# Optimization experiments

Measured on AMD Instinct MI355X. Metric: run time of the kernel, lower is better.

## Reference

```python
import jax, jax.numpy as jnp
import numpy as np

TEMPERATURE = 0.02
B, T, D = 32, 256, 128


def _l2norm(x):
    return x / jnp.linalg.norm(x, axis=-1, keepdims=True)


def setup_inputs() -> dict:
    key = jax.random.key(0)
    k1, k2, k3, k4, k5, k6 = jax.random.split(key, 6)
    query_single = _l2norm(jax.random.normal(k1, (B, D), dtype=jnp.float32))
    pos_single = _l2norm(jax.random.normal(k2, (B, D), dtype=jnp.float32))
    query_multi = _l2norm(jax.random.normal(k3, (B, T, D), dtype=jnp.float32))
    pos_multi = _l2norm(jax.random.normal(k4, (B, T, D), dtype=jnp.float32))
    # variable-length masks (at least 1 valid token each, like real tokenized batches)
    q_len = jax.random.randint(k5, (B,), T // 4, T + 1)
    p_len = jax.random.randint(k6, (B,), T // 4, T + 1)
    pos = jnp.arange(T)[None, :]
    q_mask = pos < q_len[:, None]
    p_mask = pos < p_len[:, None]
    return {
        "query_single": query_single,
        "pos_single": pos_single,
        "query_multi": query_multi,
        "pos_multi": pos_multi,
        "q_mask": q_mask,
        "p_mask": p_mask,
    }


def _late_interaction_similarity(q_tokens, q_mask, p_tokens, p_mask):
    # All-pairs token similarity: [Bq, Bp, Tq, Tp]
    sim = jnp.einsum("bqd,cpd->bcqp", q_tokens, p_tokens)
    neg = jnp.finfo(sim.dtype).min
    sim = jnp.where(p_mask[None, :, None, :], sim, neg)
    mx = jnp.max(sim, axis=-1)                       # [Bq, Bp, Tq]
    mx = jnp.where(q_mask[:, None, :], mx, 0.0)      # drop invalid query tokens
    s = jnp.sum(mx, axis=-1)                         # [Bq, Bp]
    t_i = jnp.maximum(jnp.sum(q_mask, axis=-1), 1).astype(sim.dtype)  # [Bq]
    return s / t_i[:, None]


def _diag_cross_entropy(logits):
    # labels = arange(B): standard in-batch InfoNCE
    logp = jax.nn.log_softmax(logits, axis=-1)
    return -jnp.mean(jnp.diagonal(logp))


def reference(query_single, pos_single, query_multi, pos_multi, q_mask, p_mask):
    tau = TEMPERATURE
    dense_sim = query_single @ pos_single.T                       # [B, B]
    single_loss = _diag_cross_entropy(dense_sim / tau)

    S_late = _late_interaction_similarity(query_multi, q_mask, pos_multi, p_mask)
    multi_loss = _diag_cross_entropy(S_late / tau)

    dense_probs = jax.nn.softmax(dense_sim / tau, axis=1)
    late_probs = jax.nn.softmax(S_late / tau, axis=1)
    eps = 1e-8
    kl = jnp.mean(jnp.sum(dense_probs * jnp.log((dense_probs + eps) / (late_probs + eps)), axis=1))

    total_loss = single_loss + multi_loss + kl
    return (total_loss, single_loss, multi_loss, kl)
```

## Files before the change

### kernel.cpp

```cpp
#include <hip/hip_runtime.h>
#include <hip/hip_bf16.h>

#define B_SZ 32
#define T_SZ 256
#define D_SZ 128
#define TAU_INV 50.0f

typedef __bf16 bf16x8 __attribute__((ext_vector_type(8)));
typedef float f32x4 __attribute__((ext_vector_type(4)));

__device__ __forceinline__ unsigned short f2bf(float f) {
    union { float f; unsigned int u; } v; v.f = f;
    unsigned int r = v.u + 0x7fffu + ((v.u >> 16) & 1u);
    return (unsigned short)(r >> 16);
}

__device__ __forceinline__ bool mask_is_byte(const void* m) {
    return ((const int*)m)[0] != 1;
}
__device__ __forceinline__ int mget(const void* m, int idx, bool isb) {
    return isb ? (((const unsigned char*)m)[idx] != 0) : (((const int*)m)[idx] != 0);
}

__global__ __launch_bounds__(256) void cvt_prep(
    const float* __restrict__ qsrc, const float* __restrict__ psrc,
    const void* __restrict__ qmask, const void* __restrict__ pmask,
    unsigned short* __restrict__ Qb, unsigned short* __restrict__ Pb,
    float* __restrict__ maddF, float* __restrict__ qmulF,
    int* __restrict__ p_hiA, float* __restrict__ tcntA) {
    const int tid = threadIdx.x;
    const int half = blockIdx.x >> 10;
    if (half < 2) {
        const float* s = half ? psrc : qsrc;
        unsigned short* d = half ? Pb : Qb;
        int i = ((blockIdx.x & 1023) * 256 + tid) * 4;
        float4 v = *(const float4*)(s + i);
        ushort4 o;
        o.x = f2bf(v.x); o.y = f2bf(v.y); o.z = f2bf(v.z); o.w = f2bf(v.w);
        *(ushort4*)(d + i) = o;
        return;
    }
    __shared__ int sl[4], sc[4];
    const bool isb = mask_is_byte(qmask);
    const int r = blockIdx.x - 2048;
    const int t = tid;
    const int pm = mget(pmask, r * T_SZ + t, isb);
    const int qm = mget(qmask, r * T_SZ + t, isb);
    maddF[r * T_SZ + t] = pm ? 0.0f : -1e30f;
    qmulF[r * T_SZ + t] = qm ? 1.0f : 0.0f;
    int lp = pm ? t + 1 : 0, cq = qm;
    #pragma unroll
    for (int off = 1; off < 64; off <<= 1) {
        int o = __shfl_xor(lp, off);
        lp = o > lp ? o : lp;
        cq += __shfl_xor(cq, off);
    }
    if ((tid & 63) == 0) { sl[tid >> 6] = lp; sc[tid >> 6] = cq; }
    __syncthreads();
    if (tid == 0) {
        int LP = sl[0], CQ = sc[0];
        #pragma unroll
        for (int i = 1; i < 4; ++i) { LP = sl[i] > LP ? sl[i] : LP; CQ += sc[i]; }
        p_hiA[r] = LP > 1 ? LP : 1;
        tcntA[r] = (float)(CQ > 1 ? CQ : 1);
    }
}

__global__ __launch_bounds__(512, 4) void late_sim(
    const unsigned short* __restrict__ Qbf, const unsigned short* __restrict__ Pbf,
    const float* __restrict__ maddF, const float* __restrict__ qmulF,
    const int* __restrict__ p_hiA, float* __restrict__ sraw)
{
    __shared__ __align__(16) unsigned char Plds[T_SZ * D_SZ * 2];
    __shared__ float madd[T_SZ];
    __shared__ float qmul[2][T_SZ];
    __shared__ float wsum[2][8];

    const int tid = threadIdx.x;
    const int l   = tid & 63;
    const int w   = tid >> 6;
    const int bid = blockIdx.x;
    const int xcd = bid & 7;
    const int idx = bid >> 3;
    const int bg  = xcd * 2 + (idx >> 5);
    const int c   = idx & 31;
    const int b0  = bg, b1 = bg + 16;
    const int lr  = l & 15;
    const int lg  = l >> 4;

    const int p_hi    = p_hiA[c];
    const int ptmax   = (p_hi + 15) >> 4;
    const int stiters = (p_hi + 31) >> 5;

    const int qrow = w * 32 + (l & 31);
    const bool do0 = __any(qmulF[b0 * T_SZ + qrow] > 0.0f);
    const bool do1 = __any(qmulF[b1 * T_SZ + qrow] > 0.0f);

    bf16x8 qf0[2][4] = {}, qf1[2][4] = {};
    if (do0)
        #pragma unroll
        for (int qt = 0; qt < 2; ++qt)
            #pragma unroll
            for (int k = 0; k < 4; ++k)
                qf0[qt][k] = *(const bf16x8*)(Qbf + b0 * (T_SZ * D_SZ)
                              + (w * 32 + qt * 16 + lr) * D_SZ + k * 32 + lg * 8);
    if (do1)
        #pragma unroll
        for (int qt = 0; qt < 2; ++qt)
            #pragma unroll
            for (int k = 0; k < 4; ++k)
                qf1[qt][k] = *(const bf16x8*)(Qbf + b1 * (T_SZ * D_SZ)
                              + (w * 32 + qt * 16 + lr) * D_SZ + k * 32 + lg * 8);

    {
        const unsigned short* Pc = Pbf + c * (T_SZ * D_SZ);
        for (int it = 0; it < stiters; ++it) {
            int j   = it * 512 + w * 64 + l;
            int row = j >> 4;
            int cj  = j & 15;
            const unsigned short* src = Pc + row * D_SZ + ((cj ^ (row & 7)) << 3);
            __builtin_amdgcn_global_load_lds(
                (const __attribute__((address_space(1))) unsigned int*)src,
                (__attribute__((address_space(3))) unsigned int*)(Plds + (it * 512 + w * 64) * 16),
                16, 0, 0);
        }
    }
    if (tid < 64) {
        *(float4*)(madd + tid * 4) = *(const float4*)(maddF + c * T_SZ + tid * 4);
    } else if (tid < 128) {
        int t = tid - 64;
        *(float4*)(qmul[0] + t * 4) = *(const float4*)(qmulF + b0 * T_SZ + t * 4);
    } else if (tid < 192) {
        int t = tid - 128;
        *(float4*)(qmul[1] + t * 4) = *(const float4*)(qmulF + b1 * T_SZ + t * 4);
    }
    __syncthreads();

    float r00 = -3e38f, r01 = -3e38f, r10 = -3e38f, r11 = -3e38f;

    for (int pt = 0; pt < ptmax; ++pt) {
        f32x4 a00 = {0,0,0,0}, a01 = {0,0,0,0}, a10 = {0,0,0,0}, a11 = {0,0,0,0};
        #pragma unroll
        for (int k = 0; k < 4; ++k) {
            int row = pt * 16 + lr;
            bf16x8 af = *(const bf16x8*)(Plds + row * 256 + (((k * 4 + lg) ^ (row & 7)) << 4));
            if (do0) {
                a00 = __builtin_amdgcn_mfma_f32_16x16x32_bf16(af, qf0[0][k], a00, 0, 0, 0);
                a01 = __builtin_amdgcn_mfma_f32_16x16x32_bf16(af, qf0[1][k], a01, 0, 0, 0);
            }
            if (do1) {
                a10 = __builtin_amdgcn_mfma_f32_16x16x32_bf16(af, qf1[0][k], a10, 0, 0, 0);
                a11 = __builtin_amdgcn_mfma_f32_16x16x32_bf16(af, qf1[1][k], a11, 0, 0, 0);
            }
        }
        float pm0 = madd[pt * 16 + lg * 4 + 0];
        float pm1 = madd[pt * 16 + lg * 4 + 1];
        float pm2 = madd[pt * 16 + lg * 4 + 2];
        float pm3v = madd[pt * 16 + lg * 4 + 3];
        if (do0) {
            r00 = fmaxf(r00, fmaxf(fmaxf(a00[0]+pm0, a00[1]+pm1), fmaxf(a00[2]+pm2, a00[3]+pm3v)));
            r01 = fmaxf(r01, fmaxf(fmaxf(a01[0]+pm0, a01[1]+pm1), fmaxf(a01[2]+pm2, a01[3]+pm3v)));
        }
        if (do1) {
            r10 = fmaxf(r10, fmaxf(fmaxf(a10[0]+pm0, a10[1]+pm1), fmaxf(a10[2]+pm2, a10[3]+pm3v)));
            r11 = fmaxf(r11, fmaxf(fmaxf(a11[0]+pm0, a11[1]+pm1), fmaxf(a11[2]+pm2, a11[3]+pm3v)));
        }
    }

    r00 = fmaxf(r00, __shfl_xor(r00, 16)); r00 = fmaxf(r00, __shfl_xor(r00, 32));
    r01 = fmaxf(r01, __shfl_xor(r01, 16)); r01 = fmaxf(r01, __shfl_xor(r01, 32));
    r10 = fmaxf(r10, __shfl_xor(r10, 16)); r10 = fmaxf(r10, __shfl_xor(r10, 32));
    r11 = fmaxf(r11, __shfl_xor(r11, 16)); r11 = fmaxf(r11, __shfl_xor(r11, 32));

    float t0 = r00 * qmul[0][w * 32 + lr] + r01 * qmul[0][w * 32 + 16 + lr];
    float t1 = r10 * qmul[1][w * 32 + lr] + r11 * qmul[1][w * 32 + 16 + lr];
    #pragma unroll
    for (int off = 32; off > 0; off >>= 1) {
        t0 += __shfl_down(t0, off);
        t1 += __shfl_down(t1, off);
    }
    if (l == 0) { wsum[0][w] = t0 * 0.25f; wsum[1][w] = t1 * 0.25f; }
    __syncthreads();

    if (tid == 0) {
        float s0 = 0.f, s1 = 0.f;
        #pragma unroll
        for (int ww = 0; ww < 8; ++ww) { s0 += wsum[0][ww]; s1 += wsum[1][ww]; }
        sraw[b0 * 32 + c] = s0;
        sraw[b1 * 32 + c] = s1;
    }
}

__global__ __launch_bounds__(256) void loss_final(
    const float* __restrict__ qs, const float* __restrict__ ps,
    const float* __restrict__ sraw, const float* __restrict__ tcntA,
    float* __restrict__ out)
{
    __shared__ float qsL[B_SZ * 132];
    __shared__ float psL[B_SZ * 132];
    __shared__ float dense[B_SZ * B_SZ];
    __shared__ float late[B_SZ * B_SZ];
    __shared__ float tcnt[B_SZ];
    __shared__ float rsA[B_SZ], rmA[B_SZ], rkA[B_SZ];

    const int tid = threadIdx.x;

    for (int i = tid; i < 1024; i += 256) {
        int r = i >> 5, c4 = (i & 31) * 4;
        *(float4*)(qsL + r * 132 + c4) = *(const float4*)(qs + r * D_SZ + c4);
        *(float4*)(psL + r * 132 + c4) = *(const float4*)(ps + r * D_SZ + c4);
    }
    if (tid < B_SZ) tcnt[tid] = tcntA[tid];
    __syncthreads();

    for (int idx = tid; idx < B_SZ * B_SZ; idx += 256) {
        int r = idx >> 5, cc = idx & 31;
        float s = 0.f;
        #pragma unroll
        for (int i = 0; i < D_SZ; i += 4) {
            float4 a  = *(const float4*)(qsL + r  * 132 + i);
            float4 bb = *(const float4*)(psL + cc * 132 + i);
            s += a.x * bb.x + a.y * bb.y + a.z * bb.z + a.w * bb.w;
        }
        dense[r * 32 + cc] = s;
        late[r * 32 + cc]  = sraw[idx] / tcnt[r];
    }
    __syncthreads();

    {
        const int cc = tid & 31;
        #pragma unroll
        for (int it = 0; it < 4; ++it) {
            const int r = (tid >> 5) + 8 * it;
            float xd = dense[r * 32 + cc] * TAU_INV;
            float xl = late[r * 32 + cc]  * TAU_INV;
            float md = xd, ml = xl;
            #pragma unroll
            for (int off = 16; off > 0; off >>= 1) {
                md = fmaxf(md, __shfl_xor(md, off));
                ml = fmaxf(ml, __shfl_xor(ml, off));
            }
            float sd = expf(xd - md), sl = expf(xl - ml);
            #pragma unroll
            for (int off = 16; off > 0; off >>= 1) {
                sd += __shfl_xor(sd, off);
                sl += __shfl_xor(sl, off);
            }
            float lsd = md + logf(sd);
            float lsl = ml + logf(sl);
            float pd = expf(xd - lsd);
            float pl = expf(xl - lsl);
            float klt = pd * logf((pd + 1e-8f) / (pl + 1e-8f));
            #pragma unroll
            for (int off = 16; off > 0; off >>= 1) klt += __shfl_xor(klt, off);
            if (cc == 0) rkA[r] = klt;
            if (cc == r) { rsA[r] = -(xd - lsd); rmA[r] = -(xl - lsl); }
        }
    }
    __syncthreads();

    if (tid < B_SZ) {
        float a = rsA[tid], bb = rmA[tid], c2 = rkA[tid];
        #pragma unroll
        for (int off = 16; off > 0; off >>= 1) {
            a  += __shfl_xor(a, off);
            bb += __shfl_xor(bb, off);
            c2 += __shfl_xor(c2, off);
        }
        if (tid == 0) {
            a *= (1.0f / B_SZ); bb *= (1.0f / B_SZ); c2 *= (1.0f / B_SZ);
            out[0] = a + bb + c2;
            out[1] = a;
            out[2] = bb;
            out[3] = c2;
        }
    }
}

extern "C" void kernel_launch(void* const* d_in, const int* in_sizes, int n_in,
                              void* d_out, int out_size, void* d_ws, size_t ws_size,
                              hipStream_t stream) {
    const float* qs    = (const float*)d_in[0];
    const float* ps    = (const float*)d_in[1];
    const float* qm3   = (const float*)d_in[2];
    const float* pm3   = (const float*)d_in[3];
    const void*  qmask = d_in[4];
    const void*  pmask = d_in[5];
    float* out = (float*)d_out;

    const int NTOK = B_SZ * T_SZ * D_SZ;
    unsigned short* Qbf = (unsigned short*)d_ws;
    unsigned short* Pbf = Qbf + NTOK;
    float* sraw  = (float*)(Pbf + NTOK);
    float* maddF = sraw + 1024;
    float* qmulF = maddF + B_SZ * T_SZ;
    int*   p_hiA = (int*)(qmulF + B_SZ * T_SZ);
    float* tcntA = (float*)(p_hiA + 32);

    cvt_prep<<<2080, 256, 0, stream>>>(qm3, pm3, qmask, pmask, Qbf, Pbf,
                                       maddF, qmulF, p_hiA, tcntA);
    late_sim<<<512, 512, 0, stream>>>(Qbf, Pbf, maddF, qmulF, p_hiA, sraw);
    loss_final<<<1, 256, 0, stream>>>(qs, ps, sraw, tcntA, out);
}
```

Baseline: 38.13 us.

## Split final loss kernel across one block per row with atomic accumulation

Replaces the single-block loss kernel with 32 blocks, one per query row. Each block computes its row of the dense similarity by reading global memory directly, with 8 threads per column and shuffle reductions, and handles that row's softmax, cross-entropy and KL terms. Partial results are combined with atomicAdd into outputs that are zeroed by a memset added before the kernels run. This spreads the serial tail kernel across more compute units, at the cost of an extra memset call and float atomics whose summation order is not deterministic.

```diff
diff --git a/kernel.cpp b/kernel.cpp
--- a/kernel.cpp
+++ b/kernel.cpp
@@ -191,89 +191,72 @@
     }
 }
 
-__global__ __launch_bounds__(256) void loss_final(
+__global__ __launch_bounds__(256) void loss_row(
     const float* __restrict__ qs, const float* __restrict__ ps,
     const float* __restrict__ sraw, const float* __restrict__ tcntA,
     float* __restrict__ out)
 {
-    __shared__ float qsL[B_SZ * 132];
-    __shared__ float psL[B_SZ * 132];
-    __shared__ float dense[B_SZ * B_SZ];
-    __shared__ float late[B_SZ * B_SZ];
-    __shared__ float tcnt[B_SZ];
-    __shared__ float rsA[B_SZ], rmA[B_SZ], rkA[B_SZ];
-
+    __shared__ float denseL[B_SZ], lateL[B_SZ];
+    const int r   = blockIdx.x;
     const int tid = threadIdx.x;
-
-    for (int i = tid; i < 1024; i += 256) {
-        int r = i >> 5, c4 = (i & 31) * 4;
-        *(float4*)(qsL + r * 132 + c4) = *(const float4*)(qs + r * D_SZ + c4);
-        *(float4*)(psL + r * 132 + c4) = *(const float4*)(ps + r * D_SZ + c4);
-    }
-    if (tid < B_SZ) tcnt[tid] = tcntA[tid];
-    __syncthreads();
-
-    for (int idx = tid; idx < B_SZ * B_SZ; idx += 256) {
-        int r = idx >> 5, cc = idx & 31;
+    const int cc  = tid >> 3;
+    const int j   = tid & 7;
+
+    {
+        const float4* qa = (const float4*)(qs + r  * D_SZ + j * 16);
+        const float4* pb = (const float4*)(ps + cc * D_SZ + j * 16);
         float s = 0.f;
         #pragma unroll
-        for (int i = 0; i < D_SZ; i += 4) {
-            float4 a  = *(const float4*)(qsL + r  * 132 + i);
-            float4 bb = *(const float4*)(psL + cc * 132 + i);
-            s += a.x * bb.x + a.y * bb.y + a.z * bb.z + a.w * bb.w;
-        }
-        dense[r * 32 + cc] = s;
-        late[r * 32 + cc]  = sraw[idx] / tcnt[r];
-    }
-    __syncthreads();
-
-    {
-        const int cc = tid & 31;
-        #pragma unroll
-        for (int it = 0; it < 4; ++it) {
-            const int r = (tid >> 5) + 8 * it;
-            float xd = dense[r * 32 + cc] * TAU_INV;
-            float xl = late[r * 32 + cc]  * TAU_INV;
-            float md = xd, ml = xl;
-            #pragma unroll
-            for (int off = 16; off > 0; off >>= 1) {
-                md = fmaxf(md, __shfl_xor(md, off));
-                ml = fmaxf(ml, __shfl_xor(ml, off));
-            }
-            float sd = expf(xd - md), sl = expf(xl - ml);
-            #pragma unroll
-            for (int off = 16; off > 0; off >>= 1) {
-                sd += __shfl_xor(sd, off);
-                sl += __shfl_xor(sl, off);
-            }
-            float lsd = md + logf(sd);
-            float lsl = ml + logf(sl);
-            float pd = expf(xd - lsd);
-            float pl = expf(xl - lsl);
-            float klt = pd * logf((pd + 1e-8f) / (pl + 1e-8f));
-            #pragma unroll
-            for (int off = 16; off > 0; off >>= 1) klt += __shfl_xor(klt, off);
-            if (cc == 0) rkA[r] = klt;
-            if (cc == r) { rsA[r] = -(xd - lsd); rmA[r] = -(xl - lsl); }
-        }
-    }
-    __syncthreads();
-
-    if (tid < B_SZ) {
-        float a = rsA[tid], bb = rmA[tid], c2 = rkA[tid];
-        #pragma unroll
-        for (int off = 16; off > 0; off >>= 1) {
-            a  += __shfl_xor(a, off);
-            bb += __shfl_xor(bb, off);
-            c2 += __shfl_xor(c2, off);
-        }
-        if (tid == 0) {
-            a *= (1.0f / B_SZ); bb *= (1.0f / B_SZ); c2 *= (1.0f / B_SZ);
-            out[0] = a + bb + c2;
-            out[1] = a;
-            out[2] = bb;
-            out[3] = c2;
-        }
+        for (int v = 0; v < 4; ++v) {
+            float4 q = qa[v], p = pb[v];
+            s += q.x * p.x + q.y * p.y + q.z * p.z + q.w * p.w;
+        }
+        s += __shfl_xor(s, 1);
+        s += __shfl_xor(s, 2);
+        s += __shfl_xor(s, 4);
+        if (j == 0) denseL[cc] = s;
+    }
+    if (tid < B_SZ) lateL[tid] = sraw[r * 32 + tid] / tcntA[r];
+    __syncthreads();
+
+    if (tid >= 32) return;
+    const int lane = tid;
+    float xd = denseL[lane] * TAU_INV;
+    float xl = lateL[lane]  * TAU_INV;
+    float md = xd, ml = xl;
+    #pragma unroll
+    for (int off = 16; off > 0; off >>= 1) {
+        md = fmaxf(md, __shfl_xor(md, off));
+        ml = fmaxf(ml, __shfl_xor(ml, off));
+    }
+    float sd = expf(xd - md), sl = expf(xl - ml);
+    #pragma unroll
+    for (int off = 16; off > 0; off >>= 1) {
+        sd += __shfl_xor(sd, off);
+        sl += __shfl_xor(sl, off);
+    }
+    float lsd = md + logf(sd);
+    float lsl = ml + logf(sl);
+    float pd = expf(xd - lsd);
+    float pl = expf(xl - lsl);
+    float klt = pd * logf((pd + 1e-8f) / (pl + 1e-8f));
+    #pragma unroll
+    for (int off = 16; off > 0; off >>= 1) klt += __shfl_xor(klt, off);
+
+    float logpd = xd - lsd;
+    float logpl = xl - lsl;
+    float dlogd = __shfl(logpd, r);
+    float dlogl = __shfl(logpl, r);
+
+    if (lane == 0) {
+        const float inv = 1.0f / (float)B_SZ;
+        float a = -dlogd * inv;
+        float b = -dlogl * inv;
+        float k = klt * inv;
+        atomicAdd(out + 1, a);
+        atomicAdd(out + 2, b);
+        atomicAdd(out + 3, k);
+        atomicAdd(out + 0, a + b + k);
     }
 }
 
@@ -297,8 +280,9 @@
     int*   p_hiA = (int*)(qmulF + B_SZ * T_SZ);
     float* tcntA = (float*)(p_hiA + 32);
 
+    hipMemsetAsync(out, 0, 4 * sizeof(float), stream);
     cvt_prep<<<2080, 256, 0, stream>>>(qm3, pm3, qmask, pmask, Qbf, Pbf,
                                        maddF, qmulF, p_hiA, tcntA);
     late_sim<<<512, 512, 0, stream>>>(Qbf, Pbf, maddF, qmulF, p_hiA, sraw);
-    loss_final<<<1, 256, 0, stream>>>(qs, ps, sraw, tcntA, out);
-}
+    loss_row<<<B_SZ, 256, 0, stream>>>(qs, ps, sraw, tcntA, out);
+}
```

Result: faster. 35.73 us (-6.3%).
